# Optimization experiments

Measured on AMD Instinct MI355X. Metric: run time of the kernel, lower is better.

Reference implementation:

```python
import jax, jax.numpy as jnp
import numpy as np

B, N, D, H, E, ED = 32, 256, 1024, 16, 512, 256
HD = D // H
NEG = float(np.finfo(np.float32).min)


def setup_inputs() -> dict:
    key = jax.random.key(0)
    ks = iter(jax.random.split(key, 16))
    def nrm(shape, fan_in):
        return jax.random.normal(next(ks), shape, jnp.float32) / np.sqrt(fan_in)
    return {
        "x": jax.random.normal(next(ks), (B, N, D), jnp.float32),
        "node_masks": jnp.ones((B, N), jnp.float32),
        "relation_edges": jax.random.randint(next(ks), (B, E, 2), 0, N, jnp.int64),
        "relation_masks": jnp.ones((B, E), jnp.float32),
        "relation_embeddings": jax.random.normal(next(ks), (B, E, ED), jnp.float32),
        "ln_g": jnp.ones((D,), jnp.float32), "ln_b": jnp.zeros((D,), jnp.float32),
        "Wq": nrm((D, D), D), "bq": jnp.zeros((D,), jnp.float32),
        "Wk": nrm((D, D), D), "bk": jnp.zeros((D,), jnp.float32),
        "Wv": nrm((D, D), D), "bv": jnp.zeros((D,), jnp.float32),
        "We": nrm((ED, H), ED), "be": jnp.zeros((H,), jnp.float32),
        "Wo": nrm((D, D), D), "bo": jnp.zeros((D,), jnp.float32),
        "ff_g": jnp.ones((D,), jnp.float32), "ff_b": jnp.zeros((D,), jnp.float32),
        "W1": nrm((D, 4 * D), D), "b1": jnp.zeros((4 * D,), jnp.float32),
        "W2": nrm((4 * D, D), 4 * D), "b2": jnp.zeros((D,), jnp.float32),
    }


def _ln(x, g, b):
    m = jnp.mean(x, axis=-1, keepdims=True)
    v = jnp.mean((x - m) ** 2, axis=-1, keepdims=True)
    return (x - m) / jnp.sqrt(v + 1e-5) * g + b


def reference(x, node_masks, relation_edges, relation_masks, relation_embeddings,
              ln_g, ln_b, Wq, bq, Wk, bk, Wv, bv, We, be, Wo, bo,
              ff_g, ff_b, W1, b1, W2, b2):
    residual = x
    xn = _ln(x, ln_g, ln_b)
    # [B,N,D] -> [B,H,N,HD]
    def split_heads(t):
        return t.reshape(B, N, H, HD).transpose(0, 2, 1, 3)
    q = split_heads(xn @ Wq + bq)
    k = split_heads(xn @ Wk + bk)
    v = split_heads(xn @ Wv + bv)
    attn = jnp.einsum('bhqd,bhkd->bhqk', q, k) / np.sqrt(HD)

    nb = node_masks.astype(bool)
    pair_mask = nb[:, None, :, None] & nb[:, None, None, :]  # [B,1,N,N]

    # --- scatter edge list into dense adjacency + per-head bias ---
    src = jnp.clip(relation_edges[..., 0], 0, N - 1)  # [B,E]
    dst = jnp.clip(relation_edges[..., 1], 0, N - 1)
    valid = relation_masks.astype(bool)
    # route invalid edges to a padding row/col N, sliced off afterwards
    src_w = jnp.where(valid, src, N)
    dst_w = jnp.where(valid, dst, N)
    b_idx = jnp.broadcast_to(jnp.arange(B)[:, None], (B, E))

    Np = N + 1
    adj = jnp.broadcast_to(jnp.eye(Np, dtype=bool), (B, Np, Np))
    adj = adj.at[b_idx, src_w, dst_w].set(True).at[b_idx, dst_w, src_w].set(True)
    rel_adj = adj[:, :N, :N][:, None]  # [B,1,N,N]

    eb = relation_embeddings @ We + be  # [B,E,H]
    bias = jnp.zeros((B, Np, Np, H), x.dtype)
    bias = bias.at[b_idx, src_w, dst_w].set(eb).at[b_idx, dst_w, src_w].set(eb)
    rel_bias = bias[:, :N, :N, :].transpose(0, 3, 1, 2)  # [B,H,N,N]

    attn = attn + rel_bias
    pair_mask = pair_mask & rel_adj
    attn = jnp.where(pair_mask, attn, NEG)
    attn = jax.nn.softmax(attn, axis=-1)
    attn = jnp.nan_to_num(attn)

    out = jnp.einsum('bhqk,bhkd->bhqd', attn, v).transpose(0, 2, 1, 3).reshape(B, N, D)
    x = residual + (out @ Wo + bo)
    h = _ln(x, ff_g, ff_b)
    h = jax.nn.silu(h @ W1 + b1) @ W2 + b2
    x = x + h
    return x * node_masks[..., None]
```

## Files before the change

### kernel.cpp

```cpp
#include <hip/hip_runtime.h>
#include <math.h>

#define B_  32
#define N_  256
#define D_  1024
#define H_  16
#define E_  512
#define ED_ 256
#define HD_ 64
#define QS_ 3072
#define NEG_ (-3.4028234663852886e38f)

typedef __attribute__((ext_vector_type(8))) short short8;
typedef __attribute__((ext_vector_type(4))) float f32x4;
typedef __attribute__((ext_vector_type(16))) float f32x16;
typedef unsigned short ushort_t;
typedef unsigned int uint_t;

union U16x8 { uint4 u4; ushort_t s[8]; };

static __device__ __forceinline__ ushort_t f2bf(float f) {
    uint_t u = __builtin_bit_cast(uint_t, f);
    u = (u + 0x7fff + ((u >> 16) & 1)) >> 16;
    return (ushort_t)u;
}

static __device__ __forceinline__ void gload_lds16(const void* g, void* l) {
    __builtin_amdgcn_global_load_lds(
        (const __attribute__((address_space(1))) unsigned int*)g,
        (__attribute__((address_space(3))) unsigned int*)l, 16, 0, 0);
}

__global__ __launch_bounds__(256) void ln_bf16_kernel(const float* __restrict__ x,
                                                      const float* __restrict__ g,
                                                      const float* __restrict__ b,
                                                      ushort_t* __restrict__ out) {
    int row = blockIdx.x;
    const float* xr = x + (size_t)row * D_;
    ushort_t* yr = out + (size_t)row * D_;
    __shared__ float red[256];
    int t = threadIdx.x;
    float vals[4];
    float s = 0.f;
#pragma unroll
    for (int i = 0; i < 4; ++i) { vals[i] = xr[t + i * 256]; s += vals[i]; }
    red[t] = s; __syncthreads();
    for (int off = 128; off > 0; off >>= 1) { if (t < off) red[t] += red[t + off]; __syncthreads(); }
    float mean = red[0] * (1.f / D_);
    __syncthreads();
    float vs = 0.f;
#pragma unroll
    for (int i = 0; i < 4; ++i) { float d = vals[i] - mean; vs += d * d; }
    red[t] = vs; __syncthreads();
    for (int off = 128; off > 0; off >>= 1) { if (t < off) red[t] += red[t + off]; __syncthreads(); }
    float rstd = 1.f / sqrtf(red[0] * (1.f / D_) + 1e-5f);
#pragma unroll
    for (int i = 0; i < 4; ++i) {
        int c = t + i * 256;
        yr[c] = f2bf((vals[i] - mean) * rstd * g[c] + b[c]);
    }
}

__global__ __launch_bounds__(256) void prep_kernel(
    const float* __restrict__ Wq, const float* __restrict__ Wk,
    const float* __restrict__ Wv, const float* __restrict__ Wo,
    const float* __restrict__ W1, const float* __restrict__ W2,
    const float* __restrict__ bq, const float* __restrict__ bk,
    const float* __restrict__ bv,
    ushort_t* __restrict__ qkvT, ushort_t* __restrict__ WoT,
    ushort_t* __restrict__ W1T, ushort_t* __restrict__ W2T,
    float* __restrict__ cb)
{
    int id = blockIdx.x;
    if (id >= 12288) {
        int i = (id - 12288) * 256 + threadIdx.x;
        cb[i] = (i < 1024) ? bq[i] : ((i < 2048) ? bk[i - 1024] : bv[i - 2048]);
        return;
    }
    const float* in; ushort_t* outp; int K, N, tid;
    if (id < 4096) {
        int wsel = id >> 10; tid = id & 1023; K = D_; N = D_;
        in   = (wsel == 0) ? Wq : (wsel == 1) ? Wk : (wsel == 2) ? Wv : Wo;
        outp = (wsel == 0) ? qkvT : (wsel == 1) ? qkvT + 1024 * 1024
             : (wsel == 2) ? qkvT + 2 * 1024 * 1024 : WoT;
    } else if (id < 8192) { tid = id - 4096; K = D_; N = 4 * D_; in = W1; outp = W1T; }
    else                  { tid = id - 8192; K = 4 * D_; N = D_; in = W2; outp = W2T; }
    int tilesX = N >> 5;
    int n0 = (tid % tilesX) * 32, k0 = (tid / tilesX) * 32;

    __shared__ float tile[32][33];
    int tx = threadIdx.x & 31, ty = threadIdx.x >> 5;
#pragma unroll
    for (int r = 0; r < 4; ++r)
        tile[ty + r * 8][tx] = in[(size_t)(k0 + ty + r * 8) * N + n0 + tx];
    __syncthreads();
#pragma unroll
    for (int r = 0; r < 4; ++r)
        outp[(size_t)(n0 + ty + r * 8) * K + k0 + tx] = f2bf(tile[tx][ty + r * 8]);
}

__global__ __launch_bounds__(256) void eb_kernel(const float* __restrict__ re,
                                                 const float* __restrict__ We,
                                                 const float* __restrict__ be,
                                                 float* __restrict__ eb) {
    __shared__ float rs[16 * 256];
    __shared__ float wl[256 * 16];
    int t = threadIdx.x;
    int be0 = blockIdx.x * 16;
#pragma unroll
    for (int i = 0; i < 16; ++i) wl[t + i * 256] = We[t + i * 256];
#pragma unroll
    for (int i = 0; i < 16; ++i) rs[t + i * 256] = re[(size_t)be0 * 256 + t + i * 256];
    __syncthreads();
    int el = t >> 4, h = t & 15;
    float s = be[h];
#pragma unroll 8
    for (int i = 0; i < 256; ++i) s += rs[el * 256 + i] * wl[i * 16 + h];
    eb[(size_t)(be0 + el) * 16 + h] = s;
}

__global__ void scatter_kernel(const int* __restrict__ edges, const float* __restrict__ emask,
                               int* __restrict__ prio) {
    int idx = blockIdx.x * blockDim.x + threadIdx.x;
    if (idx >= B_ * E_) return;
    if (emask[idx] == 0.f) return;
    int b = idx / E_, e = idx % E_;
    int s = edges[2 * idx], d = edges[2 * idx + 1];
    s = min(max(s, 0), N_ - 1);
    d = min(max(d, 0), N_ - 1);
    int* base = prio + (size_t)b * N_ * N_;
    atomicMax(&base[s * N_ + d], e);
    atomicMax(&base[d * N_ + s], e + E_);
}

template<int MODE>
__global__ __launch_bounds__(256) void gemm_bf16(
    const ushort_t* __restrict__ A, const ushort_t* __restrict__ BT,
    const float* __restrict__ bias, const float* __restrict__ res,
    const float* __restrict__ nm, void* __restrict__ Cout,
    int M, int N, int K)
{
    __shared__ ushort_t As[128 * 64];
    __shared__ ushort_t Bs[128 * 64];
    int t = threadIdx.x;
    int lane = t & 63;
    int l31 = lane & 31, lh = lane >> 5;
    int w = t >> 6;
    int wr = (w >> 1) * 64, wc = (w & 1) * 64;

    int bid = blockIdx.x;
    int xcd = bid & 7;
    int lid = bid >> 3;
    int st  = lid >> 5;
    int ls  = lid & 31;
    int brow = xcd * 8 + (ls >> 2);
    int bcol = st * 4 + (ls & 3);
    int row0 = brow * 128, col0 = bcol * 128;

    const ushort_t* Ag = A + (size_t)row0 * K;
    const ushort_t* Bg = BT + (size_t)col0 * K;
    int srow = t >> 3;
    int slot = t & 7;
    int sc = (slot ^ (srow & 7)) * 8;

    f32x16 acc[2][2];
#pragma unroll
    for (int i = 0; i < 2; ++i)
#pragma unroll
        for (int j = 0; j < 2; ++j)
#pragma unroll
            for (int r = 0; r < 16; ++r) acc[i][j][r] = 0.f;

    for (int k0 = 0; k0 < K; k0 += 64) {
#pragma unroll
        for (int i = 0; i < 4; ++i) {
            gload_lds16(Ag + (size_t)(i * 32 + srow) * K + k0 + sc, (char*)As + i * 4096 + t * 16);
            gload_lds16(Bg + (size_t)(i * 32 + srow) * K + k0 + sc, (char*)Bs + i * 4096 + t * 16);
        }
        __syncthreads();
#pragma unroll
        for (int ks = 0; ks < 4; ++ks) {
            short8 af[2], bfr[2];
#pragma unroll
            for (int it = 0; it < 2; ++it) {
                int m = wr + it * 32 + l31;
                int x = ((ks * 2 + lh) ^ (m & 7)) * 16;
                af[it] = *(const short8*)((const char*)As + m * 128 + x);
            }
#pragma unroll
            for (int jt = 0; jt < 2; ++jt) {
                int n = wc + jt * 32 + l31;
                int x = ((ks * 2 + lh) ^ (n & 7)) * 16;
                bfr[jt] = *(const short8*)((const char*)Bs + n * 128 + x);
            }
#pragma unroll
            for (int it = 0; it < 2; ++it)
#pragma unroll
                for (int jt = 0; jt < 2; ++jt)
                    acc[it][jt] = __builtin_amdgcn_mfma_f32_32x32x16_bf16(af[it], bfr[jt], acc[it][jt], 0, 0, 0);
        }
        __syncthreads();
    }

#pragma unroll
    for (int it = 0; it < 2; ++it) {
#pragma unroll
        for (int jt = 0; jt < 2; ++jt) {
            int col = col0 + wc + jt * 32 + l31;
            float bcol_b = bias[col];
#pragma unroll
            for (int reg = 0; reg < 16; ++reg) {
                int row = row0 + wr + it * 32 + (reg & 3) + 8 * (reg >> 2) + 4 * lh;
                float v = acc[it][jt][reg] + bcol_b;
                if (MODE == 0) {
                    ((ushort_t*)Cout)[(size_t)row * N + col] = f2bf(v);
                } else {
                    v = v / (1.f + __expf(-v));
                    ((ushort_t*)Cout)[(size_t)row * N + col] = f2bf(v);
                }
            }
        }
    }
}

template<int MODE>
__global__ __launch_bounds__(256) void gemm_res(
    const ushort_t* __restrict__ A, const ushort_t* __restrict__ BT,
    const float* __restrict__ bias, const float* __restrict__ res,
    const float* __restrict__ nm, void* __restrict__ Cout,
    int M, int N, int K)
{
    __shared__ ushort_t As[2][128 * 64];
    __shared__ ushort_t Bs[2][128 * 64];
    int t = threadIdx.x;
    int lane = t & 63;
    int l31 = lane & 31, lh = lane >> 5;
    int w = t >> 6;
    int wr = (w >> 1) * 64, wc = (w & 1) * 64;

    int bid = blockIdx.x;
    int xcd = bid & 7;
    int lid = bid >> 3;
    int st  = lid >> 5;
    int ls  = lid & 31;
    int brow = xcd * 8 + (ls >> 2);
    int bcol = st * 4 + (ls & 3);
    int row0 = brow * 128, col0 = bcol * 128;

    const ushort_t* Ag = A + (size_t)row0 * K;
    const ushort_t* Bg = BT + (size_t)col0 * K;
    int srow = t >> 3;
    int slot = t & 7;
    int sc = (slot ^ (srow & 7)) * 8;

    f32x16 acc[2][2];
#pragma unroll
    for (int i = 0; i < 2; ++i)
#pragma unroll
        for (int j = 0; j < 2; ++j)
#pragma unroll
            for (int r = 0; r < 16; ++r) acc[i][j][r] = 0.f;

    for (int k0 = 0; k0 < K; k0 += 128) {
#pragma unroll
        for (int p = 0; p < 2; ++p)
#pragma unroll
            for (int i = 0; i < 4; ++i) {
                gload_lds16(Ag + (size_t)(i * 32 + srow) * K + k0 + p * 64 + sc,
                            (char*)As + p * 16384 + i * 4096 + t * 16);
                gload_lds16(Bg + (size_t)(i * 32 + srow) * K + k0 + p * 64 + sc,
                            (char*)Bs + p * 16384 + i * 4096 + t * 16);
            }
        __syncthreads();
#pragma unroll
        for (int ks8 = 0; ks8 < 8; ++ks8) {
            const char* Ab = (const char*)As + (ks8 >> 2) * 16384;
            const char* Bb = (const char*)Bs + (ks8 >> 2) * 16384;
            int kk = ks8 & 3;
            short8 af[2], bfr[2];
#pragma unroll
            for (int it = 0; it < 2; ++it) {
                int m = wr + it * 32 + l31;
                int x = ((kk * 2 + lh) ^ (m & 7)) * 16;
                af[it] = *(const short8*)(Ab + m * 128 + x);
            }
#pragma unroll
            for (int jt = 0; jt < 2; ++jt) {
                int n = wc + jt * 32 + l31;
                int x = ((kk * 2 + lh) ^ (n & 7)) * 16;
                bfr[jt] = *(const short8*)(Bb + n * 128 + x);
            }
#pragma unroll
            for (int it = 0; it < 2; ++it)
#pragma unroll
                for (int jt = 0; jt < 2; ++jt)
                    acc[it][jt] = __builtin_amdgcn_mfma_f32_32x32x16_bf16(af[it], bfr[jt], acc[it][jt], 0, 0, 0);
        }
        __syncthreads();
    }

#pragma unroll
    for (int it = 0; it < 2; ++it) {
#pragma unroll
        for (int jt = 0; jt < 2; ++jt) {
            int col = col0 + wc + jt * 32 + l31;
            float bcol_b = bias[col];
#pragma unroll
            for (int reg = 0; reg < 16; ++reg) {
                int row = row0 + wr + it * 32 + (reg & 3) + 8 * (reg >> 2) + 4 * lh;
                float v = acc[it][jt][reg] + bcol_b;
                if (MODE == 1) {
                    ((float*)Cout)[(size_t)row * N + col] = v + res[(size_t)row * N + col];
                } else {
                    v = (v + res[(size_t)row * N + col]) * nm[row];
                    ((float*)Cout)[(size_t)row * N + col] = v;
                }
            }
        }
    }
}

__global__ __launch_bounds__(256) void gemm_sk3(
    const ushort_t* __restrict__ A, const ushort_t* __restrict__ BT,
    const float* __restrict__ bias, const float* __restrict__ res,
    const float* __restrict__ nm, float* __restrict__ Cout,
    int M, int N, int K)
{
    __shared__ ushort_t As[128 * 64];
    __shared__ ushort_t Bs[128 * 64];
    int t = threadIdx.x;
    int lane = t & 63;
    int l31 = lane & 31, lh = lane >> 5;
    int w = t >> 6;
    int wr = (w >> 1) * 64, wc = (w & 1) * 64;

    int bid = blockIdx.x;
    int kh  = bid >> 9;
    bid &= 511;
    int xcd = bid & 7;
    int lid = bid >> 3;
    int st  = lid >> 5;
    int ls  = lid & 31;
    int brow = xcd * 8 + (ls >> 2);
    int bcol = st * 4 + (ls & 3);
    int row0 = brow * 128, col0 = bcol * 128;

    int khalf = K >> 1;
    const ushort_t* Ag = A + (size_t)row0 * K + kh * khalf;
    const ushort_t* Bg = BT + (size_t)col0 * K + kh * khalf;
    int srow = t >> 3;
    int slot = t & 7;
    int sc = (slot ^ (srow & 7)) * 8;

    f32x16 acc[2][2];
#pragma unroll
    for (int i = 0; i < 2; ++i)
#pragma unroll
        for (int j = 0; j < 2; ++j)
#pragma unroll
            for (int r = 0; r < 16; ++r) acc[i][j][r] = 0.f;

    for (int k0 = 0; k0 < khalf; k0 += 64) {
#pragma unroll
        for (int i = 0; i < 4; ++i) {
            gload_lds16(Ag + (size_t)(i * 32 + srow) * K + k0 + sc, (char*)As + i * 4096 + t * 16);
            gload_lds16(Bg + (size_t)(i * 32 + srow) * K + k0 + sc, (char*)Bs + i * 4096 + t * 16);
        }
        __syncthreads();
#pragma unroll
        for (int ks = 0; ks < 4; ++ks) {
            short8 af[2], bfr[2];
#pragma unroll
            for (int it = 0; it < 2; ++it) {
                int m = wr + it * 32 + l31;
                int x = ((ks * 2 + lh) ^ (m & 7)) * 16;
                af[it] = *(const short8*)((const char*)As + m * 128 + x);
            }
#pragma unroll
            for (int jt = 0; jt < 2; ++jt) {
                int n = wc + jt * 32 + l31;
                int x = ((ks * 2 + lh) ^ (n & 7)) * 16;
                bfr[jt] = *(const short8*)((const char*)Bs + n * 128 + x);
            }
#pragma unroll
            for (int it = 0; it < 2; ++it)
#pragma unroll
                for (int jt = 0; jt < 2; ++jt)
                    acc[it][jt] = __builtin_amdgcn_mfma_f32_32x32x16_bf16(af[it], bfr[jt], acc[it][jt], 0, 0, 0);
        }
        __syncthreads();
    }

#pragma unroll
    for (int it = 0; it < 2; ++it) {
#pragma unroll
        for (int jt = 0; jt < 2; ++jt) {
            int col = col0 + wc + jt * 32 + l31;
            float bcol_b = bias[col];
#pragma unroll
            for (int reg = 0; reg < 16; ++reg) {
                int row = row0 + wr + it * 32 + (reg & 3) + 8 * (reg >> 2) + 4 * lh;
                float v = acc[it][jt][reg];
                if (kh == 0) v += bcol_b + res[(size_t)row * N + col];
                v *= nm[row];
                atomicAdd(&Cout[(size_t)row * N + col], v);
            }
        }
    }
}

template<int NBN>
__global__ __launch_bounds__(512) void gemm256(
    const ushort_t* __restrict__ A, const ushort_t* __restrict__ BT,
    const float* __restrict__ bias, ushort_t* __restrict__ Cout,
    int M, int N, int K)
{
    __shared__ ushort_t As[2][2][128 * 64];
    __shared__ ushort_t Bs[2][2][128 * 64];

    int t = threadIdx.x;
    int lane = t & 63;
    int w = t >> 6;
    int wm = w >> 2, wn = w & 3;
    int c2 = lane & 15, quad = lane >> 4;

    int bid = blockIdx.x;
    int xcd = bid & 7, lid = bid >> 3;
    int brow = xcd * 4 + (lid & 3);
    int bcol = lid >> 2;
    int row0 = brow * 256, col0 = bcol * 256;

    const ushort_t* Ag = A + (size_t)row0 * K;
    const ushort_t* Bg = BT + (size_t)col0 * K;

    int srow = t >> 3, slot = t & 7;
    int sc = (slot ^ (srow & 7)) * 8;

    auto stage = [&](int buf, int hh, int kt) {
        const ushort_t* g = (hh < 2) ? Ag : Bg;
        int h = hh & 1;
        char* l = (hh < 2) ? (char*)&As[buf][h][0] : (char*)&Bs[buf][h][0];
        gload_lds16(g + (size_t)(h * 128 + srow) * K + kt * 64 + sc, l + t * 16);
        gload_lds16(g + (size_t)(h * 128 + 64 + srow) * K + kt * 64 + sc, l + 8192 + t * 16);
    };

    f32x4 acc[8][4];
#pragma unroll
    for (int a_ = 0; a_ < 8; ++a_)
#pragma unroll
        for (int b_ = 0; b_ < 4; ++b_)
#pragma unroll
            for (int r = 0; r < 4; ++r) acc[a_][b_][r] = 0.f;

    int T = K >> 6;
    stage(0, 0, 0); stage(0, 1, 0); stage(0, 2, 0); stage(0, 3, 0);
    if (T > 1) { stage(1, 2, 1); stage(1, 3, 1); stage(1, 0, 1); }

    const int bhalf = wn >> 1, bco = (wn & 1) * 64;

    for (int tau = 0; tau < T; ++tau) {
        int bc = tau & 1;
        const char* Ab = (const char*)&As[bc][wm][0];
        const char* Bb = (const char*)&Bs[bc][bhalf][0];
        short8 bfr[4][2];
#pragma unroll
        for (int q = 0; q < 4; ++q) {
            if (q == 0) {
                if (tau == T - 1) asm volatile("s_waitcnt vmcnt(0)" ::: "memory");
                else              asm volatile("s_waitcnt vmcnt(6)" ::: "memory");
                __builtin_amdgcn_s_barrier();
                __builtin_amdgcn_sched_barrier(0);
            }
            short8 afr[2][2];
#pragma unroll
            for (int it = 0; it < 2; ++it)
#pragma unroll
                for (int ks = 0; ks < 2; ++ks) {
                    int fr = q * 32 + it * 16 + c2;
                    afr[it][ks] = *(const short8*)(Ab + fr * 128 + (((ks * 4 + quad) ^ (fr & 7)) * 16));
                }
            if (q == 0) {
#pragma unroll
                for (int jt = 0; jt < 4; ++jt)
#pragma unroll
                    for (int ks = 0; ks < 2; ++ks) {
                        int fr = bco + jt * 16 + c2;
                        bfr[jt][ks] = *(const short8*)(Bb + fr * 128 + (((ks * 4 + quad) ^ (fr & 7)) * 16));
                    }
            }
            if (q == 0) { if (tau + 1 < T) stage(bc ^ 1, 1, tau + 1); }
            else if (tau + 2 < T) stage(bc, (q == 1) ? 2 : (q == 2) ? 3 : 0, tau + 2);

            asm volatile("s_waitcnt lgkmcnt(0)" ::: "memory");
            __builtin_amdgcn_sched_barrier(0);
            __builtin_amdgcn_s_setprio(1);
#pragma unroll
            for (int it = 0; it < 2; ++it)
#pragma unroll
                for (int jt = 0; jt < 4; ++jt) {
                    acc[q * 2 + it][jt] = __builtin_amdgcn_mfma_f32_16x16x32_bf16(
                        afr[it][0], bfr[jt][0], acc[q * 2 + it][jt], 0, 0, 0);
                    acc[q * 2 + it][jt] = __builtin_amdgcn_mfma_f32_16x16x32_bf16(
                        afr[it][1], bfr[jt][1], acc[q * 2 + it][jt], 0, 0, 0);
                }
            __builtin_amdgcn_s_setprio(0);
            __builtin_amdgcn_sched_barrier(0);
            __builtin_amdgcn_s_barrier();
        }
    }

#pragma unroll
    for (int q = 0; q < 4; ++q)
#pragma unroll
        for (int it = 0; it < 2; ++it) {
            int row = row0 + wm * 128 + q * 32 + it * 16 + quad * 4;
#pragma unroll
            for (int jt = 0; jt < 4; ++jt) {
                int col = col0 + wn * 64 + jt * 16 + c2;
                float bc_ = bias[col];
#pragma unroll
                for (int r = 0; r < 4; ++r) {
                    float v = acc[q * 2 + it][jt][r] + bc_;
                    v = v / (1.f + __expf(-v));
                    Cout[(size_t)(row + r) * N + col] = f2bf(v);
                }
            }
        }
}

__global__ __launch_bounds__(256, 2) void attn_mfma_kernel(
    const ushort_t* __restrict__ qkv, const int* __restrict__ prio,
    const float* __restrict__ eb, const float* __restrict__ nm,
    ushort_t* __restrict__ out)
{
    int xb = blockIdx.x;
    int bid = (xb & 7) * 256 + (xb >> 3);
    int h = bid & 15, qt = (bid >> 4) & 3, b = bid >> 6;
    int t = threadIdx.x;

    __shared__ ushort_t Ks[256 * 72];
    __shared__ ushort_t Vt[64 * 264];

    int lane = t & 63, c = lane & 15, quad = lane >> 4;
    int w = t >> 6;
    int qbase = qt * 64 + w * 16 + quad * 4;

    int pr[16][4];
    const int* prp = prio + ((size_t)(b * N_ + qbase)) * N_ + c;
#pragma unroll
    for (int j = 0; j < 16; ++j)
#pragma unroll
        for (int r = 0; r < 4; ++r)
            pr[j][r] = prp[(size_t)r * N_ + j * 16];

    float nmq[4];
#pragma unroll
    for (int r = 0; r < 4; ++r) nmq[r] = nm[b * N_ + qbase + r];
    float nmk[16];
#pragma unroll
    for (int j = 0; j < 16; ++j) nmk[j] = nm[b * N_ + j * 16 + c];

    const ushort_t* qg = qkv + ((size_t)(b * N_ + qt * 64 + w * 16 + c)) * QS_ + h * HD_;
    short8 aq0 = *(const short8*)(const void*)(qg + quad * 8);
    short8 aq1 = *(const short8*)(const void*)(qg + 32 + quad * 8);

    int lr = t >> 3, lc = (t & 7) * 8;
    const ushort_t* kg = qkv + ((size_t)(b * N_)) * QS_ + 1024 + h * HD_;
#pragma unroll
    for (int r = 0; r < 256; r += 32)
        *(uint4*)&Ks[(lr + r) * 72 + lc] = *(const uint4*)&kg[(size_t)(lr + r) * QS_ + lc];
    const ushort_t* vg = qkv + ((size_t)(b * N_)) * QS_ + 2048 + h * HD_;
#pragma unroll
    for (int r = 0; r < 256; r += 32) {
        U16x8 uu; uu.u4 = *(const uint4*)&vg[(size_t)(lr + r) * QS_ + lc];
#pragma unroll
        for (int i = 0; i < 8; ++i)
            Vt[(lc + i) * 264 + lr + r] = uu.s[i];
    }

    const float* ebb = eb + (size_t)b * E_ * H_ + h;
    float badd[16][4];
#pragma unroll
    for (int j = 0; j < 16; ++j) {
        int key = j * 16 + c;
#pragma unroll
        for (int r = 0; r < 4; ++r) {
            int p = pr[j][r];
            float bias = 0.f;
            bool adj = (key == qbase + r);
            if (p >= 0) {
                int e = (p >= E_) ? p - E_ : p;
                bias = ebb[(size_t)e * H_];
                adj = true;
            }
            bool ok = adj && (nmq[r] != 0.f) && (nmk[j] != 0.f);
            badd[j][r] = ok ? bias : -3.0e38f;
        }
    }
    __syncthreads();

    f32x4 z = {0.f, 0.f, 0.f, 0.f};
    f32x4 acc[16];
#pragma unroll
    for (int j = 0; j < 16; ++j) acc[j] = z;
    __builtin_amdgcn_s_setprio(1);
#pragma unroll
    for (int j = 0; j < 16; ++j) {
        short8 b0 = *(const short8*)(const void*)(Ks + (j * 16 + c) * 72 + quad * 8);
        short8 b1 = *(const short8*)(const void*)(Ks + (j * 16 + c) * 72 + 32 + quad * 8);
        acc[j] = __builtin_amdgcn_mfma_f32_16x16x32_bf16(aq0, b0, acc[j], 0, 0, 0);
        acc[j] = __builtin_amdgcn_mfma_f32_16x16x32_bf16(aq1, b1, acc[j], 0, 0, 0);
    }
    __builtin_amdgcn_s_setprio(0);

#pragma unroll
    for (int j = 0; j < 16; ++j)
#pragma unroll
        for (int r = 0; r < 4; ++r)
            acc[j][r] = acc[j][r] * 0.125f + badd[j][r];

    float inv[4];
#pragma unroll
    for (int r = 0; r < 4; ++r) {
        float m = acc[0][r];
#pragma unroll
        for (int j = 1; j < 16; ++j) m = fmaxf(m, acc[j][r]);
        m = fmaxf(m, __shfl_xor(m, 1));
        m = fmaxf(m, __shfl_xor(m, 2));
        m = fmaxf(m, __shfl_xor(m, 4));
        m = fmaxf(m, __shfl_xor(m, 8));
        float s = 0.f;
#pragma unroll
        for (int j = 0; j < 16; ++j) {
            float p = __expf(acc[j][r] - m);
            acc[j][r] = p;
            s += p;
        }
        s += __shfl_xor(s, 1);
        s += __shfl_xor(s, 2);
        s += __shfl_xor(s, 4);
        s += __shfl_xor(s, 8);
        inv[r] = 1.f / s;
    }

    __syncthreads();
    ushort_t* Ps = Ks;
#pragma unroll
    for (int j = 0; j < 16; ++j)
#pragma unroll
        for (int r = 0; r < 4; ++r)
            Ps[(w * 16 + quad * 4 + r) * 264 + j * 16 + c] = f2bf(acc[j][r] * inv[r]);
    asm volatile("s_waitcnt lgkmcnt(0)" ::: "memory");

    f32x4 oc[4];
#pragma unroll
    for (int dt = 0; dt < 4; ++dt) oc[dt] = z;
    __builtin_amdgcn_s_setprio(1);
#pragma unroll
    for (int k0 = 0; k0 < 256; k0 += 32) {
        short8 ap = *(const short8*)(const void*)(Ps + (w * 16 + c) * 264 + k0 + quad * 8);
#pragma unroll
        for (int dt = 0; dt < 4; ++dt) {
            short8 bv = *(const short8*)(const void*)(Vt + (dt * 16 + c) * 264 + k0 + quad * 8);
            oc[dt] = __builtin_amdgcn_mfma_f32_16x16x32_bf16(ap, bv, oc[dt], 0, 0, 0);
        }
    }
    __builtin_amdgcn_s_setprio(0);
    ushort_t* og = out + ((size_t)(b * N_ + qt * 64 + w * 16)) * D_ + h * HD_;
#pragma unroll
    for (int dt = 0; dt < 4; ++dt)
#pragma unroll
        for (int r = 0; r < 4; ++r)
            og[(size_t)(quad * 4 + r) * D_ + dt * 16 + c] = f2bf(oc[dt][r]);
}

extern "C" void kernel_launch(void* const* d_in, const int* in_sizes, int n_in,
                              void* d_out, int out_size, void* d_ws, size_t ws_size,
                              hipStream_t stream) {
    const float* x     = (const float*)d_in[0];
    const float* nm    = (const float*)d_in[1];
    const int*   edges = (const int*)d_in[2];
    const float* emask = (const float*)d_in[3];
    const float* remb  = (const float*)d_in[4];
    const float* ln_g  = (const float*)d_in[5];
    const float* ln_b  = (const float*)d_in[6];
    const float* Wq = (const float*)d_in[7];  const float* bq = (const float*)d_in[8];
    const float* Wk = (const float*)d_in[9];  const float* bk = (const float*)d_in[10];
    const float* Wv = (const float*)d_in[11]; const float* bv = (const float*)d_in[12];
    const float* We = (const float*)d_in[13]; const float* be = (const float*)d_in[14];
    const float* Wo = (const float*)d_in[15]; const float* bo = (const float*)d_in[16];
    const float* ff_g = (const float*)d_in[17]; const float* ff_b = (const float*)d_in[18];
    const float* W1 = (const float*)d_in[19]; const float* b1 = (const float*)d_in[20];
    const float* W2 = (const float*)d_in[21]; const float* b2 = (const float*)d_in[22];
    float* out = (float*)d_out;

    char* ws = (char*)d_ws;
    const size_t MB = 1ll << 20;
    int*      prio = (int*)ws;
    float*    ebuf = (float*)(ws + 8 * MB);
    ushort_t* xn   = (ushort_t*)(ws + 9 * MB);
    float*    x2   = (float*)(ws + 25 * MB);
    ushort_t* hn   = (ushort_t*)(ws + 57 * MB);
    ushort_t* qkv  = (ushort_t*)(ws + 73 * MB);
    ushort_t* mid  = qkv;
    ushort_t* qkvT = (ushort_t*)(ws + 137 * MB);
    ushort_t* WoT  = (ushort_t*)(ws + 143 * MB);
    ushort_t* W1T  = (ushort_t*)(ws + 145 * MB);
    ushort_t* W2T  = (ushort_t*)(ws + 153 * MB);
    float*    cb   = (float*)(ws + 161 * MB);
    ushort_t* aout = xn;

    const int M = B_ * N_;

    (void)hipMemsetAsync(out, 0, (size_t)M * D_ * sizeof(float), stream);
    (void)hipMemsetAsync(prio, 0xFF, (size_t)B_ * N_ * N_ * sizeof(int), stream);
    eb_kernel<<<B_ * E_ / 16, 256, 0, stream>>>(remb, We, be, ebuf);
    scatter_kernel<<<(B_ * E_ + 255) / 256, 256, 0, stream>>>(edges, emask, prio);

    prep_kernel<<<12300, 256, 0, stream>>>(Wq, Wk, Wv, Wo, W1, W2, bq, bk, bv,
                                           qkvT, WoT, W1T, W2T, cb);

    ln_bf16_kernel<<<M, 256, 0, stream>>>(x, ln_g, ln_b, xn);

    gemm_bf16<0><<<24 * 64, 256, 0, stream>>>(xn, qkvT, cb, nullptr, nullptr, qkv, M, QS_, D_);

    attn_mfma_kernel<<<B_ * H_ * 4, 256, 0, stream>>>(qkv, prio, ebuf, nm, aout);

    gemm_res<1><<<8 * 64, 256, 0, stream>>>(aout, WoT, bo, x, nullptr, x2, M, D_, D_);
    ln_bf16_kernel<<<M, 256, 0, stream>>>(x2, ff_g, ff_b, hn);

    gemm256<16><<<512, 512, 0, stream>>>(hn, W1T, b1, mid, M, 4 * D_, D_);
    gemm_sk3<<<1024, 256, 0, stream>>>(mid, W2T, b2, x2, nm, out, M, D_, 4 * D_);
}
```

Baseline: 555.9 us.

## Replace split-K atomic W2 GEMM with 4-stage prefetch pipeline; vectorize layernorm

The final FFN down-projection GEMM no longer splits K across two blocks that merge with atomicAdd into a zeroed output. It now runs the full K per block through a 4-buffer LDS ring with 32-wide K tiles, using explicit vmcnt waits and global-to-LDS prefetch three tiles ahead, and writes results directly. This removes the output memset and the atomic traffic, at the cost of half as many blocks and less parallelism. The layernorm kernel is also vectorized to float4 loads and ushort4 stores.

```diff
diff --git a/kernel.cpp b/kernel.cpp
--- a/kernel.cpp
+++ b/kernel.cpp
@@ -36,29 +36,29 @@
                                                       const float* __restrict__ b,
                                                       ushort_t* __restrict__ out) {
     int row = blockIdx.x;
-    const float* xr = x + (size_t)row * D_;
+    const float4* xr = (const float4*)(x + (size_t)row * D_);
     ushort_t* yr = out + (size_t)row * D_;
     __shared__ float red[256];
     int t = threadIdx.x;
-    float vals[4];
-    float s = 0.f;
-#pragma unroll
-    for (int i = 0; i < 4; ++i) { vals[i] = xr[t + i * 256]; s += vals[i]; }
+    float4 v4 = xr[t];
+    float s = v4.x + v4.y + v4.z + v4.w;
     red[t] = s; __syncthreads();
     for (int off = 128; off > 0; off >>= 1) { if (t < off) red[t] += red[t + off]; __syncthreads(); }
     float mean = red[0] * (1.f / D_);
     __syncthreads();
-    float vs = 0.f;
-#pragma unroll
-    for (int i = 0; i < 4; ++i) { float d = vals[i] - mean; vs += d * d; }
-    red[t] = vs; __syncthreads();
+    float d0 = v4.x - mean, d1 = v4.y - mean, d2 = v4.z - mean, d3 = v4.w - mean;
+    red[t] = d0 * d0 + d1 * d1 + d2 * d2 + d3 * d3;
+    __syncthreads();
     for (int off = 128; off > 0; off >>= 1) { if (t < off) red[t] += red[t + off]; __syncthreads(); }
     float rstd = 1.f / sqrtf(red[0] * (1.f / D_) + 1e-5f);
-#pragma unroll
-    for (int i = 0; i < 4; ++i) {
-        int c = t + i * 256;
-        yr[c] = f2bf((vals[i] - mean) * rstd * g[c] + b[c]);
-    }
+    float4 g4 = ((const float4*)g)[t];
+    float4 b4 = ((const float4*)b)[t];
+    ushort4 o;
+    o.x = f2bf(d0 * rstd * g4.x + b4.x);
+    o.y = f2bf(d1 * rstd * g4.y + b4.y);
+    o.z = f2bf(d2 * rstd * g4.z + b4.z);
+    o.w = f2bf(d3 * rstd * g4.w + b4.w);
+    *(ushort4*)(yr + t * 4) = o;
 }
 
 __global__ __launch_bounds__(256) void prep_kernel(
@@ -320,14 +320,14 @@
     }
 }
 
-__global__ __launch_bounds__(256) void gemm_sk3(
+__global__ __launch_bounds__(256) void gemm_pf3(
     const ushort_t* __restrict__ A, const ushort_t* __restrict__ BT,
     const float* __restrict__ bias, const float* __restrict__ res,
     const float* __restrict__ nm, float* __restrict__ Cout,
     int M, int N, int K)
 {
-    __shared__ ushort_t As[128 * 64];
-    __shared__ ushort_t Bs[128 * 64];
+    __shared__ ushort_t As[4][128 * 32];
+    __shared__ ushort_t Bs[4][128 * 32];
     int t = threadIdx.x;
     int lane = t & 63;
     int l31 = lane & 31, lh = lane >> 5;
@@ -335,8 +335,6 @@
     int wr = (w >> 1) * 64, wc = (w & 1) * 64;
 
     int bid = blockIdx.x;
-    int kh  = bid >> 9;
-    bid &= 511;
     int xcd = bid & 7;
     int lid = bid >> 3;
     int st  = lid >> 5;
@@ -345,12 +343,11 @@
     int bcol = st * 4 + (ls & 3);
     int row0 = brow * 128, col0 = bcol * 128;
 
-    int khalf = K >> 1;
-    const ushort_t* Ag = A + (size_t)row0 * K + kh * khalf;
-    const ushort_t* Bg = BT + (size_t)col0 * K + kh * khalf;
-    int srow = t >> 3;
-    int slot = t & 7;
-    int sc = (slot ^ (srow & 7)) * 8;
+    const ushort_t* Ag = A + (size_t)row0 * K;
+    const ushort_t* Bg = BT + (size_t)col0 * K;
+    int srow = t >> 2;
+    int slot = t & 3;
+    int sc = (slot ^ (srow & 3)) * 8;
 
     f32x16 acc[2][2];
 #pragma unroll
@@ -360,27 +357,51 @@
 #pragma unroll
             for (int r = 0; r < 16; ++r) acc[i][j][r] = 0.f;
 
-    for (int k0 = 0; k0 < khalf; k0 += 64) {
-#pragma unroll
-        for (int i = 0; i < 4; ++i) {
-            gload_lds16(Ag + (size_t)(i * 32 + srow) * K + k0 + sc, (char*)As + i * 4096 + t * 16);
-            gload_lds16(Bg + (size_t)(i * 32 + srow) * K + k0 + sc, (char*)Bs + i * 4096 + t * 16);
-        }
-        __syncthreads();
-#pragma unroll
-        for (int ks = 0; ks < 4; ++ks) {
+    auto stage = [&](int bf, int kt) {
+        gload_lds16(Ag + (size_t)srow * K + kt * 32 + sc, (char*)As[bf] + t * 16);
+        gload_lds16(Ag + (size_t)(64 + srow) * K + kt * 32 + sc, (char*)As[bf] + 4096 + t * 16);
+        gload_lds16(Bg + (size_t)srow * K + kt * 32 + sc, (char*)Bs[bf] + t * 16);
+        gload_lds16(Bg + (size_t)(64 + srow) * K + kt * 32 + sc, (char*)Bs[bf] + 4096 + t * 16);
+    };
+
+    int T = K >> 5;
+    stage(0, 0); stage(1, 1); stage(2, 2);
+
+    for (int tau = 0; tau < T; ++tau) {
+        int buf = tau & 3;
+        if (tau + 2 < T)      asm volatile("s_waitcnt vmcnt(8)" ::: "memory");
+        else if (tau + 1 < T) asm volatile("s_waitcnt vmcnt(4)" ::: "memory");
+        else                  asm volatile("s_waitcnt vmcnt(0)" ::: "memory");
+        __builtin_amdgcn_s_barrier();
+        __builtin_amdgcn_sched_barrier(0);
+
+        const char* Ab = (const char*)As[buf];
+        const char* Bb = (const char*)Bs[buf];
+#pragma unroll
+        for (int ks = 0; ks < 2; ++ks) {
+            if (tau + 3 < T) {
+                int nb = (tau + 3) & 3;
+                int kb = (tau + 3) * 32;
+                if (ks == 0) {
+                    gload_lds16(Ag + (size_t)srow * K + kb + sc, (char*)As[nb] + t * 16);
+                    gload_lds16(Ag + (size_t)(64 + srow) * K + kb + sc, (char*)As[nb] + 4096 + t * 16);
+                } else {
+                    gload_lds16(Bg + (size_t)srow * K + kb + sc, (char*)Bs[nb] + t * 16);
+                    gload_lds16(Bg + (size_t)(64 + srow) * K + kb + sc, (char*)Bs[nb] + 4096 + t * 16);
+                }
+            }
             short8 af[2], bfr[2];
 #pragma unroll
             for (int it = 0; it < 2; ++it) {
                 int m = wr + it * 32 + l31;
-                int x = ((ks * 2 + lh) ^ (m & 7)) * 16;
-                af[it] = *(const short8*)((const char*)As + m * 128 + x);
+                int x = ((ks * 2 + lh) ^ (m & 3)) * 16;
+                af[it] = *(const short8*)(Ab + m * 64 + x);
             }
 #pragma unroll
             for (int jt = 0; jt < 2; ++jt) {
                 int n = wc + jt * 32 + l31;
-                int x = ((ks * 2 + lh) ^ (n & 7)) * 16;
-                bfr[jt] = *(const short8*)((const char*)Bs + n * 128 + x);
+                int x = ((ks * 2 + lh) ^ (n & 3)) * 16;
+                bfr[jt] = *(const short8*)(Bb + n * 64 + x);
             }
 #pragma unroll
             for (int it = 0; it < 2; ++it)
@@ -388,7 +409,6 @@
                 for (int jt = 0; jt < 2; ++jt)
                     acc[it][jt] = __builtin_amdgcn_mfma_f32_32x32x16_bf16(af[it], bfr[jt], acc[it][jt], 0, 0, 0);
         }
-        __syncthreads();
     }
 
 #pragma unroll
@@ -400,10 +420,9 @@
 #pragma unroll
             for (int reg = 0; reg < 16; ++reg) {
                 int row = row0 + wr + it * 32 + (reg & 3) + 8 * (reg >> 2) + 4 * lh;
-                float v = acc[it][jt][reg];
-                if (kh == 0) v += bcol_b + res[(size_t)row * N + col];
-                v *= nm[row];
-                atomicAdd(&Cout[(size_t)row * N + col], v);
+                float v = acc[it][jt][reg] + bcol_b;
+                v = (v + res[(size_t)row * N + col]) * nm[row];
+                Cout[(size_t)row * N + col] = v;
             }
         }
     }
@@ -712,7 +731,6 @@
 
     const int M = B_ * N_;
 
-    (void)hipMemsetAsync(out, 0, (size_t)M * D_ * sizeof(float), stream);
     (void)hipMemsetAsync(prio, 0xFF, (size_t)B_ * N_ * N_ * sizeof(int), stream);
     eb_kernel<<<B_ * E_ / 16, 256, 0, stream>>>(remb, We, be, ebuf);
     scatter_kernel<<<(B_ * E_ + 255) / 256, 256, 0, stream>>>(edges, emask, prio);
@@ -730,5 +748,5 @@
     ln_bf16_kernel<<<M, 256, 0, stream>>>(x2, ff_g, ff_b, hn);
 
     gemm256<16><<<512, 512, 0, stream>>>(hn, W1T, b1, mid, M, 4 * D_, D_);
-    gemm_sk3<<<1024, 256, 0, stream>>>(mid, W2T, b2, x2, nm, out, M, D_, 4 * D_);
-}
+    gemm_pf3<<<8 * 64, 256, 0, stream>>>(mid, W2T, b2, x2, nm, out, M, D_, 4 * D_);
+}
```

Result: faster. 530.4 us (-4.6%).
